# Performance work log

Hardware: AMD Instinct MI355X
Metric: run time of the kernel (lower is better)

## Reference

```python
import jax, jax.numpy as jnp
import numpy as np

NEG_SLOPE = 0.2  # PyG GATConv default leaky_relu slope


def gat_layer(x, W, a_src, a_dst, b):
    # x: [B, N, Fin]; W: [Fin, H*C]; a_src/a_dst: [H, C]; b: [H*C]
    # Dense-block equivalent of PyG GATConv on a fully-connected block graph
    # (self loops included), concat=True.
    B, N, Fin = x.shape
    H, C = a_src.shape
    h = jnp.einsum('bnf,fhc->bnhc', x, W.reshape(Fin, H, C))  # [B,N,H,C]
    ls = jnp.einsum('bnhc,hc->bnh', h, a_src)  # alpha_src per node
    ld = jnp.einsum('bnhc,hc->bnh', h, a_dst)  # alpha_dst per node
    # logits[i, j] = leaky_relu(alpha_dst[i] + alpha_src[j]); softmax over j
    logits = jax.nn.leaky_relu(ld[:, :, None, :] + ls[:, None, :, :], NEG_SLOPE)  # [B,i,j,H]
    attn = jax.nn.softmax(logits, axis=2)
    out = jnp.einsum('bijh,bjhc->bihc', attn, h).reshape(B, N, H * C)
    return out + b


def setup_inputs() -> dict:
    key = jax.random.key(0)
    ks = jax.random.split(key, 12)
    bs, R, Nc, enc = 8, 256, 64, 31
    H, hid, out = 8, 64, 32
    Fin = 1 + enc  # 32
    p = lambda k, shape: jax.random.normal(k, shape, jnp.float32) * 0.05
    return {
        'xs': jax.random.normal(ks[0], (bs, R, Nc), jnp.float32),
        'pos_enc': jax.random.normal(ks[1], (bs, Nc, enc), jnp.float32),
        'W1': p(ks[2], (Fin, H * hid)), 'as1': p(ks[3], (H, hid)), 'ad1': p(ks[4], (H, hid)),
        'b1': jnp.zeros((H * hid,), jnp.float32),
        'W2': p(ks[5], (H * hid, H * hid)), 'as2': p(ks[6], (H, hid)), 'ad2': p(ks[7], (H, hid)),
        'b2': jnp.zeros((H * hid,), jnp.float32),
        'W3': p(ks[8], (H * hid, H * out)), 'as3': p(ks[9], (H, out)), 'ad3': p(ks[10], (H, out)),
        'b3': jnp.zeros((H * out,), jnp.float32),
    }


def reference(xs, pos_enc, W1, as1, ad1, b1, W2, as2, ad2, b2, W3, as3, ad3, b3):
    bs, R, Nc = xs.shape
    enc = pos_enc.shape[-1]
    pe = jnp.broadcast_to(pos_enc[:, None], (bs, R, Nc, enc))
    x = jnp.concatenate([xs[..., None], pe], axis=-1)  # [bs,R,Nc,1+enc]
    x = x.reshape(bs * R, Nc, 1 + enc)  # independent fully-connected blocks
    x = gat_layer(x, W1, as1, ad1, b1)
    x = gat_layer(x, W2, as2, ad2, b2)
    x = gat_layer(x, W3, as3, ad3, b3)
    out = x.reshape(bs, R, Nc, -1).mean(axis=2)  # mean over num_xs
    return out
```

## Files before the change

kernel.cpp:

```cpp
#include <hip/hip_runtime.h>
#include <hip/hip_bf16.h>

typedef __hip_bfloat16 bf16;
typedef unsigned int uint32;
typedef __attribute__((ext_vector_type(8))) short short8;
typedef __attribute__((ext_vector_type(4))) float float4v;
typedef __attribute__((ext_vector_type(16))) float float16v;

#define THREADS 512
#define LDX 520
#define LDE 68

__device__ __forceinline__ bf16 f2b(float x) { return __float2bfloat16(x); }
__device__ __forceinline__ uint32 packbf2(float x, float y) {
  union { __hip_bfloat162 b; uint32 u; } cv;
  cv.b = __float22bfloat162_rn(make_float2(x, y));
  return cv.u;
}

__global__ void convw_all(const float* __restrict__ W1,
                          const float* __restrict__ W2,
                          const float* __restrict__ W3, bf16* __restrict__ dst) {
  int o = blockIdx.x * 256 + threadIdx.x;
  if (o >= 409600) return;
  const float* W;
  int Mlog, loc;
  if (o < 16384) { W = W1; Mlog = 9; loc = o; }
  else if (o < 278528) { W = W2; Mlog = 9; loc = o - 16384; }
  else { W = W3; Mlog = 8; loc = o - 278528; }
  int j = loc & 7, q = (loc >> 3) & 1, rest = loc >> 4;
  int M = 1 << Mlog;
  int n = rest & (M - 1), kb = rest >> Mlog;
  int k = kb * 16 + q * 8 + j;
  dst[o] = f2b(W[(size_t)k * M + n]);
}

__global__ void convE_all(
    const float* __restrict__ W1, const float* __restrict__ as1, const float* __restrict__ ad1,
    const float* __restrict__ W2, const float* __restrict__ as2, const float* __restrict__ ad2,
    const float* __restrict__ W3, const float* __restrict__ as3, const float* __restrict__ ad3,
    bf16* __restrict__ dstE) {
  int o = blockIdx.x * 256 + threadIdx.x;
  if (o >= 16896) return;
  const float *W, *as_, *ad_;
  int M, C, loc;
  if (o < 512) { loc = o; W = W1; as_ = as1; ad_ = ad1; M = 512; C = 64; }
  else if (o < 8704) { loc = o - 512; W = W2; as_ = as2; ad_ = ad2; M = 512; C = 64; }
  else { loc = o - 8704; W = W3; as_ = as3; ad_ = ad3; M = 256; C = 32; }
  int j = loc & 7, kc = (loc >> 3) & 3, n = (loc >> 5) & 15, ks = loc >> 9;
  int k = ks * 32 + kc * 8 + j;
  int head = n & 7;
  const float* a = (n < 8) ? as_ : ad_;
  float s = 0.f;
  for (int c = 0; c < C; ++c)
    s += W[(size_t)k * M + head * C + c] * a[head * C + c];
  dstE[o] = f2b(s);
}

template <int K, int M, int C, bool LAST>
__device__ __forceinline__ void gat_layer(
    int t, const bf16* __restrict__ Wswz, const bf16* __restrict__ WE,
    const float* __restrict__ bias, bf16* sX, float* sE) {
  constexpr int NCT = C / 32;
  constexpr int KS16 = K / 16;
  constexpr int KSE = K / 32;
  const int lane = t & 63;
  const int hu = __builtin_amdgcn_readfirstlane(t >> 6);
  const int c = lane & 31, q = lane >> 5;
  const int ln16 = lane & 15, kq16 = lane >> 4;
  const int colbase = hu * C;

  if (hu < 4) {
    float4v acce = (float4v)0.f;
#pragma unroll
    for (int ks = 0; ks < KSE; ++ks) {
      short8 afrE = *(const short8*)(sX + (hu * 16 + ln16) * LDX + ks * 32 + kq16 * 8);
      short8 efr = *(const short8*)(WE + ks * 512 + ln16 * 32 + kq16 * 8);
      acce = __builtin_amdgcn_mfma_f32_16x16x32_bf16(afrE, efr, acce, 0, 0, 0);
    }
    *(float4v*)(sE + ln16 * LDE + hu * 16 + kq16 * 4) = acce;
  }

  uint32 Ppk[NCT][4][4];
  {
    float16v acc[2][NCT];
#pragma unroll
    for (int rt = 0; rt < 2; ++rt)
#pragma unroll
      for (int ct = 0; ct < NCT; ++ct) acc[rt][ct] = (float16v)0.f;
    const bf16* ap = sX + c * LDX + q * 8;
    const bf16* bp = Wswz + ((colbase + c) * 2 + q) * 8;
#pragma unroll 4
    for (int ks = 0; ks < KS16; ++ks) {
      short8 afr[2];
      afr[0] = *(const short8*)(ap + ks * 16);
      afr[1] = *(const short8*)(ap + 32 * LDX + ks * 16);
      short8 bfr[NCT];
#pragma unroll
      for (int ct = 0; ct < NCT; ++ct)
        bfr[ct] = *(const short8*)(bp + (size_t)ks * (M * 16) + ct * 32 * 16);
#pragma unroll
      for (int rt = 0; rt < 2; ++rt)
#pragma unroll
        for (int ct = 0; ct < NCT; ++ct)
          acc[rt][ct] = __builtin_amdgcn_mfma_f32_32x32x16_bf16(
              afr[rt], bfr[ct], acc[rt][ct], 0, 0, 0);
    }
#pragma unroll
    for (int rt = 0; rt < 2; ++rt)
#pragma unroll
      for (int ct = 0; ct < NCT; ++ct)
#pragma unroll
        for (int tp = 0; tp < 2; ++tp) {
          Ppk[ct][rt * 2 + tp][0] = packbf2(acc[rt][ct][8 * tp + 0], acc[rt][ct][8 * tp + 1]);
          Ppk[ct][rt * 2 + tp][1] = packbf2(acc[rt][ct][8 * tp + 2], acc[rt][ct][8 * tp + 3]);
          Ppk[ct][rt * 2 + tp][2] = packbf2(acc[rt][ct][8 * tp + 4], acc[rt][ct][8 * tp + 5]);
          Ppk[ct][rt * 2 + tp][3] = packbf2(acc[rt][ct][8 * tp + 6], acc[rt][ct][8 * tp + 7]);
        }
  }

  __syncthreads();

  const float* lsrow = sE + hu * LDE;
  const float* ldrow = sE + (8 + hu) * LDE;
  short8 pfr[2][4];
#pragma unroll
  for (int rt = 0; rt < 2; ++rt) {
    const float ldi = ldrow[rt * 32 + c];
    float pe_[4][8];
    float rsum = 0.f;
#pragma unroll
    for (int tt = 0; tt < 4; ++tt) {
      float4 v0 = *(const float4*)(lsrow + tt * 16 + q * 8);
      float4 v1 = *(const float4*)(lsrow + tt * 16 + q * 8 + 4);
      float ls8[8] = {v0.x, v0.y, v0.z, v0.w, v1.x, v1.y, v1.z, v1.w};
#pragma unroll
      for (int jj = 0; jj < 8; ++jj) {
        float tv = ldi + ls8[jj];
        float l = fmaxf(tv, 0.2f * tv);
        float e = __expf(l);
        pe_[tt][jj] = e;
        rsum += e;
      }
    }
    rsum += __shfl_xor(rsum, 32, 64);
    const float ri = 1.0f / rsum;
#pragma unroll
    for (int tt = 0; tt < 4; ++tt) {
      union { uint32 d[4]; short8 s; } w;
#pragma unroll
      for (int jp = 0; jp < 4; ++jp)
        w.d[jp] = packbf2(pe_[tt][2 * jp] * ri, pe_[tt][2 * jp + 1] * ri);
      pfr[rt][tt] = w.s;
    }
  }

#pragma unroll
  for (int ct = 0; ct < NCT; ++ct) {
    short8 hfr[4];
#pragma unroll
    for (int tt = 0; tt < 4; ++tt) {
      uint32 U0 = Ppk[ct][tt][0], U1 = Ppk[ct][tt][1];
      uint32 V0 = Ppk[ct][tt][2], V1 = Ppk[ct][tt][3];
      uint32 X0 = q ? U0 : V0;
      uint32 X1 = q ? U1 : V1;
      uint32 R0 = (uint32)__shfl_xor((int)X0, 32, 64);
      uint32 R1 = (uint32)__shfl_xor((int)X1, 32, 64);
      union { uint32 d[4]; short8 s; } u;
      u.d[0] = q ? R0 : U0;
      u.d[1] = q ? R1 : U1;
      u.d[2] = q ? V0 : R0;
      u.d[3] = q ? V1 : R1;
      hfr[tt] = u.s;
    }
    float16v oacc[2];
    oacc[0] = (float16v)0.f;
    oacc[1] = (float16v)0.f;
#pragma unroll
    for (int tt = 0; tt < 4; ++tt) {
      oacc[0] = __builtin_amdgcn_mfma_f32_32x32x16_bf16(pfr[0][tt], hfr[tt], oacc[0], 0, 0, 0);
      oacc[1] = __builtin_amdgcn_mfma_f32_32x32x16_bf16(pfr[1][tt], hfr[tt], oacc[1], 0, 0, 0);
    }
    const float bv = bias[colbase + ct * 32 + c];
#pragma unroll
    for (int rt = 0; rt < 2; ++rt)
#pragma unroll
      for (int r = 0; r < 16; ++r) {
        float val = oacc[rt][r] + bv;
        int row = rt * 32 + (r & 3) + 8 * (r >> 2) + 4 * q;
        if constexpr (LAST)
          ((float*)sX)[row * 260 + colbase + ct * 32 + c] = val;
        else
          sX[row * LDX + colbase + ct * 32 + c] = f2b(val);
      }
  }
  __syncthreads();
}

__global__ __launch_bounds__(THREADS, 4) void gat3_mfma(
    const float* __restrict__ xs, const float* __restrict__ pe,
    const bf16* __restrict__ W1s, const bf16* __restrict__ WE1,
    const float* __restrict__ b1, const bf16* __restrict__ W2s,
    const bf16* __restrict__ WE2, const float* __restrict__ b2,
    const bf16* __restrict__ W3s, const bf16* __restrict__ WE3,
    const float* __restrict__ b3, float* __restrict__ out) {
  extern __shared__ char smem[];
  bf16* sX = (bf16*)smem;
  float* sE = (float*)(smem + 66560);

  const int t = threadIdx.x;
  const int blk = blockIdx.x;
  const int bidx = blk >> 8;

  for (int idx = t; idx < 64 * 32; idx += THREADS) {
    int n = idx >> 5, f = idx & 31;
    float v = (f == 0) ? xs[blk * 64 + n] : pe[(bidx * 64 + n) * 31 + (f - 1)];
    sX[n * LDX + f] = f2b(v);
  }
  __syncthreads();

  gat_layer<32, 512, 64, false>(t, W1s, WE1, b1, sX, sE);
  gat_layer<512, 512, 64, false>(t, W2s, WE2, b2, sX, sE);
  gat_layer<512, 256, 32, true>(t, W3s, WE3, b3, sX, sE);

  const float* xf = (const float*)sX;
  if (t < 256) {
    float s = 0.f;
#pragma unroll 8
    for (int i = 0; i < 64; ++i) s += xf[i * 260 + t];
    out[blk * 256 + t] = s * 0.015625f;
  }
}

extern "C" void kernel_launch(void* const* d_in, const int* in_sizes, int n_in,
                              void* d_out, int out_size, void* d_ws, size_t ws_size,
                              hipStream_t stream) {
  const float* xs = (const float*)d_in[0];
  const float* pe = (const float*)d_in[1];
  const float* W1 = (const float*)d_in[2];
  const float* as1 = (const float*)d_in[3];
  const float* ad1 = (const float*)d_in[4];
  const float* b1 = (const float*)d_in[5];
  const float* W2 = (const float*)d_in[6];
  const float* as2 = (const float*)d_in[7];
  const float* ad2 = (const float*)d_in[8];
  const float* b2 = (const float*)d_in[9];
  const float* W3 = (const float*)d_in[10];
  const float* as3 = (const float*)d_in[11];
  const float* ad3 = (const float*)d_in[12];
  const float* b3 = (const float*)d_in[13];

  bf16* Wall = (bf16*)d_ws;
  bf16* WEall = Wall + 409600;
  bf16* W1s = Wall;
  bf16* W2s = Wall + 16384;
  bf16* W3s = Wall + 278528;
  bf16* WE1 = WEall;
  bf16* WE2 = WEall + 512;
  bf16* WE3 = WEall + 8704;

  convw_all<<<dim3(1600), dim3(256), 0, stream>>>(W1, W2, W3, Wall);
  convE_all<<<dim3(66), dim3(256), 0, stream>>>(W1, as1, ad1, W2, as2, ad2,
                                                W3, as3, ad3, WEall);

  const size_t smem = 70912;
  (void)hipFuncSetAttribute((const void*)gat3_mfma,
                            hipFuncAttributeMaxDynamicSharedMemorySize,
                            (int)smem);
  gat3_mfma<<<dim3(2048), dim3(THREADS), smem, stream>>>(
      xs, pe, W1s, WE1, b1, W2s, WE2, b2, W3s, WE3, b3, (float*)d_out);
}
```

Baseline: 249.7 us.

## Fold final mean into attention weights and defer softmax normalization

For the last layer, the attention-times-features matmul followed by a mean over nodes is replaced by column-summed attention weights (mean of softmax rows) dotted with the projected features, which removes that layer's output MFMA and the fp32 staging and reduction through shared memory. For the earlier layers, the softmax division moves after the attention matmul: unnormalized exponentials are packed to bf16 and each output row is scaled by a reciprocal row sum kept in shared memory. This recomputes the exponentials twice in the last layer and raises shared memory per block, which may affect occupancy.

```diff
diff --git a/kernel.cpp b/kernel.cpp
--- a/kernel.cpp
+++ b/kernel.cpp
@@ -60,7 +60,8 @@
 template <int K, int M, int C, bool LAST>
 __device__ __forceinline__ void gat_layer(
     int t, const bf16* __restrict__ Wswz, const bf16* __restrict__ WE,
-    const float* __restrict__ bias, bf16* sX, float* sE) {
+    const float* __restrict__ bias, bf16* sX, float* sE, float* sRi,
+    float* sW, float* __restrict__ outg, int blk) {
   constexpr int NCT = C / 32;
   constexpr int KS16 = K / 16;
   constexpr int KSE = K / 32;
@@ -123,78 +124,128 @@
 
   const float* lsrow = sE + hu * LDE;
   const float* ldrow = sE + (8 + hu) * LDE;
-  short8 pfr[2][4];
-#pragma unroll
-  for (int rt = 0; rt < 2; ++rt) {
-    const float ldi = ldrow[rt * 32 + c];
-    float pe_[4][8];
-    float rsum = 0.f;
-#pragma unroll
-    for (int tt = 0; tt < 4; ++tt) {
-      float4 v0 = *(const float4*)(lsrow + tt * 16 + q * 8);
-      float4 v1 = *(const float4*)(lsrow + tt * 16 + q * 8 + 4);
-      float ls8[8] = {v0.x, v0.y, v0.z, v0.w, v1.x, v1.y, v1.z, v1.w};
-#pragma unroll
-      for (int jj = 0; jj < 8; ++jj) {
-        float tv = ldi + ls8[jj];
-        float l = fmaxf(tv, 0.2f * tv);
-        float e = __expf(l);
-        pe_[tt][jj] = e;
-        rsum += e;
-      }
-    }
-    rsum += __shfl_xor(rsum, 32, 64);
-    const float ri = 1.0f / rsum;
-#pragma unroll
-    for (int tt = 0; tt < 4; ++tt) {
-      union { uint32 d[4]; short8 s; } w;
-#pragma unroll
-      for (int jp = 0; jp < 4; ++jp)
-        w.d[jp] = packbf2(pe_[tt][2 * jp] * ri, pe_[tt][2 * jp + 1] * ri);
-      pfr[rt][tt] = w.s;
-    }
+
+  if constexpr (!LAST) {
+    short8 pfr[2][4];
+#pragma unroll
+    for (int rt = 0; rt < 2; ++rt) {
+      const float ldi = ldrow[rt * 32 + c];
+      float rsum = 0.f;
+#pragma unroll
+      for (int tt = 0; tt < 4; ++tt) {
+        float4 v0 = *(const float4*)(lsrow + tt * 16 + q * 8);
+        float4 v1 = *(const float4*)(lsrow + tt * 16 + q * 8 + 4);
+        float ls8[8] = {v0.x, v0.y, v0.z, v0.w, v1.x, v1.y, v1.z, v1.w};
+        float pe8[8];
+#pragma unroll
+        for (int jj = 0; jj < 8; ++jj) {
+          float tv = ldi + ls8[jj];
+          float l = fmaxf(tv, 0.2f * tv);
+          float e = __expf(l);
+          pe8[jj] = e;
+          rsum += e;
+        }
+        union { uint32 d[4]; short8 s; } w;
+#pragma unroll
+        for (int jp = 0; jp < 4; ++jp)
+          w.d[jp] = packbf2(pe8[2 * jp], pe8[2 * jp + 1]);
+        pfr[rt][tt] = w.s;
+      }
+      rsum += __shfl_xor(rsum, 32, 64);
+      if (q == 0) sRi[hu * 64 + rt * 32 + c] = 1.0f / rsum;
+    }
+
+#pragma unroll
+    for (int ct = 0; ct < NCT; ++ct) {
+      short8 hfr[4];
+#pragma unroll
+      for (int tt = 0; tt < 4; ++tt) {
+        uint32 U0 = Ppk[ct][tt][0], U1 = Ppk[ct][tt][1];
+        uint32 V0 = Ppk[ct][tt][2], V1 = Ppk[ct][tt][3];
+        uint32 X0 = q ? U0 : V0;
+        uint32 X1 = q ? U1 : V1;
+        uint32 R0 = (uint32)__shfl_xor((int)X0, 32, 64);
+        uint32 R1 = (uint32)__shfl_xor((int)X1, 32, 64);
+        union { uint32 d[4]; short8 s; } u;
+        u.d[0] = q ? R0 : U0;
+        u.d[1] = q ? R1 : U1;
+        u.d[2] = q ? V0 : R0;
+        u.d[3] = q ? V1 : R1;
+        hfr[tt] = u.s;
+      }
+      float16v oacc[2];
+      oacc[0] = (float16v)0.f;
+      oacc[1] = (float16v)0.f;
+#pragma unroll
+      for (int tt = 0; tt < 4; ++tt) {
+        oacc[0] = __builtin_amdgcn_mfma_f32_32x32x16_bf16(pfr[0][tt], hfr[tt], oacc[0], 0, 0, 0);
+        oacc[1] = __builtin_amdgcn_mfma_f32_32x32x16_bf16(pfr[1][tt], hfr[tt], oacc[1], 0, 0, 0);
+      }
+      const float bv = bias[colbase + ct * 32 + c];
+#pragma unroll
+      for (int rt = 0; rt < 2; ++rt)
+#pragma unroll
+        for (int g = 0; g < 4; ++g) {
+          float4 rv = *(const float4*)(sRi + hu * 64 + rt * 32 + 8 * g + 4 * q);
+          float rva[4] = {rv.x, rv.y, rv.z, rv.w};
+#pragma unroll
+          for (int m = 0; m < 4; ++m) {
+            float val = oacc[rt][4 * g + m] * rva[m] + bv;
+            int row = rt * 32 + m + 8 * g + 4 * q;
+            sX[row * LDX + colbase + ct * 32 + c] = f2b(val);
+          }
+        }
+    }
+    __syncthreads();
+  } else {
+    {
+      const float ldi = ldrow[lane];
+      float rsum = 0.f;
+#pragma unroll
+      for (int g = 0; g < 16; ++g) {
+        float4 v = *(const float4*)(lsrow + g * 4);
+        float va[4] = {v.x, v.y, v.z, v.w};
+#pragma unroll
+        for (int m = 0; m < 4; ++m) {
+          float tv = ldi + va[m];
+          float l = fmaxf(tv, 0.2f * tv);
+          rsum += __expf(l);
+        }
+      }
+      sRi[hu * 64 + lane] = 1.0f / rsum;
+    }
+    {
+      const float lsj = lsrow[lane];
+      float csum = 0.f;
+#pragma unroll
+      for (int g = 0; g < 16; ++g) {
+        float4 dv = *(const float4*)(ldrow + g * 4);
+        float4 rv = *(const float4*)(sRi + hu * 64 + g * 4);
+        float da[4] = {dv.x, dv.y, dv.z, dv.w};
+        float ra[4] = {rv.x, rv.y, rv.z, rv.w};
+#pragma unroll
+        for (int m = 0; m < 4; ++m) {
+          float tv = da[m] + lsj;
+          float l = fmaxf(tv, 0.2f * tv);
+          csum += __expf(l) * ra[m];
+        }
+      }
+      sW[hu * 64 + lane] = csum * 0.015625f;
+    }
+    float accv = 0.f;
+#pragma unroll
+    for (int idx = 0; idx < 4; ++idx)
+#pragma unroll
+      for (int d = 0; d < 4; ++d) {
+        int row = (idx >> 1) * 32 + 16 * (idx & 1) + 8 * (d >> 1) + 4 * q + 2 * (d & 1);
+        float2 w2 = *(const float2*)(sW + hu * 64 + row);
+        uint32 u = Ppk[0][idx][d];
+        accv += w2.x * __uint_as_float(u << 16) +
+                w2.y * __uint_as_float(u & 0xffff0000u);
+      }
+    accv += __shfl_xor(accv, 32, 64);
+    if (q == 0) outg[blk * 256 + hu * 32 + c] = accv + bias[hu * 32 + c];
   }
-
-#pragma unroll
-  for (int ct = 0; ct < NCT; ++ct) {
-    short8 hfr[4];
-#pragma unroll
-    for (int tt = 0; tt < 4; ++tt) {
-      uint32 U0 = Ppk[ct][tt][0], U1 = Ppk[ct][tt][1];
-      uint32 V0 = Ppk[ct][tt][2], V1 = Ppk[ct][tt][3];
-      uint32 X0 = q ? U0 : V0;
-      uint32 X1 = q ? U1 : V1;
-      uint32 R0 = (uint32)__shfl_xor((int)X0, 32, 64);
-      uint32 R1 = (uint32)__shfl_xor((int)X1, 32, 64);
-      union { uint32 d[4]; short8 s; } u;
-      u.d[0] = q ? R0 : U0;
-      u.d[1] = q ? R1 : U1;
-      u.d[2] = q ? V0 : R0;
-      u.d[3] = q ? V1 : R1;
-      hfr[tt] = u.s;
-    }
-    float16v oacc[2];
-    oacc[0] = (float16v)0.f;
-    oacc[1] = (float16v)0.f;
-#pragma unroll
-    for (int tt = 0; tt < 4; ++tt) {
-      oacc[0] = __builtin_amdgcn_mfma_f32_32x32x16_bf16(pfr[0][tt], hfr[tt], oacc[0], 0, 0, 0);
-      oacc[1] = __builtin_amdgcn_mfma_f32_32x32x16_bf16(pfr[1][tt], hfr[tt], oacc[1], 0, 0, 0);
-    }
-    const float bv = bias[colbase + ct * 32 + c];
-#pragma unroll
-    for (int rt = 0; rt < 2; ++rt)
-#pragma unroll
-      for (int r = 0; r < 16; ++r) {
-        float val = oacc[rt][r] + bv;
-        int row = rt * 32 + (r & 3) + 8 * (r >> 2) + 4 * q;
-        if constexpr (LAST)
-          ((float*)sX)[row * 260 + colbase + ct * 32 + c] = val;
-        else
-          sX[row * LDX + colbase + ct * 32 + c] = f2b(val);
-      }
-  }
-  __syncthreads();
 }
 
 __global__ __launch_bounds__(THREADS, 4) void gat3_mfma(
@@ -207,6 +258,8 @@
   extern __shared__ char smem[];
   bf16* sX = (bf16*)smem;
   float* sE = (float*)(smem + 66560);
+  float* sRi = (float*)(smem + 70912);
+  float* sW = (float*)(smem + 72960);
 
   const int t = threadIdx.x;
   const int blk = blockIdx.x;
@@ -219,17 +272,9 @@
   }
   __syncthreads();
 
-  gat_layer<32, 512, 64, false>(t, W1s, WE1, b1, sX, sE);
-  gat_layer<512, 512, 64, false>(t, W2s, WE2, b2, sX, sE);
-  gat_layer<512, 256, 32, true>(t, W3s, WE3, b3, sX, sE);
-
-  const float* xf = (const float*)sX;
-  if (t < 256) {
-    float s = 0.f;
-#pragma unroll 8
-    for (int i = 0; i < 64; ++i) s += xf[i * 260 + t];
-    out[blk * 256 + t] = s * 0.015625f;
-  }
+  gat_layer<32, 512, 64, false>(t, W1s, WE1, b1, sX, sE, sRi, sW, out, blk);
+  gat_layer<512, 512, 64, false>(t, W2s, WE2, b2, sX, sE, sRi, sW, out, blk);
+  gat_layer<512, 256, 32, true>(t, W3s, WE3, b3, sX, sE, sRi, sW, out, blk);
 }
 
 extern "C" void kernel_launch(void* const* d_in, const int* in_sizes, int n_in,
@@ -263,7 +308,7 @@
   convE_all<<<dim3(66), dim3(256), 0, stream>>>(W1, as1, ad1, W2, as2, ad2,
                                                 W3, as3, ad3, WEall);
 
-  const size_t smem = 70912;
+  const size_t smem = 75008;
   (void)hipFuncSetAttribute((const void*)gat3_mfma,
                             hipFuncAttributeMaxDynamicSharedMemorySize,
                             (int)smem);
```

Result: slower. 273.4 us (+9.5%).
